# Performance work log

Hardware: AMD Instinct MI355X
Metric: run time of the kernel (lower is better)

The kernel has to match this reference:

```python
import jax, jax.numpy as jnp
import numpy as np
from jax.scipy.special import gammaln

# ---- constants matching init_kwargs ----
D = 64            # num_nodes
K = 64            # DiBS latent rank (k = d default)
P = 32            # n_particles
N_MC = 16         # MC graph samples for score-function grad estimator
PROJ = 128        # proj_dims
N = 2048          # observations
H = 5.0           # h_latent (Frobenius squared-exponential kernel bandwidth)
ALPHA = 0.2       # alpha_linear * t  (single SVGD step)
STEP = 0.005      # SVGD step size
ALPHA_MU = 1.0
ALPHA_LAMBD = float(D + 2)
THETA_MU = 0.0
P_EDGE = 4.0 / (D - 1)          # Erdos-Renyi edge prob (~2 expected edges/node)
LATENT_STD = 1.0 / np.sqrt(K)   # DiBS default latent prior std


def bge_log_marginal(g, data, mu0, alpha_mu, alpha_lambd):
    """BGe log marginal likelihood log p(data | G) for 0/1 adjacency g [d,d]."""
    n, d = data.shape
    small_t = alpha_mu * (alpha_lambd - d - 1.0) / (alpha_mu + 1.0)
    xbar = data.mean(0)
    xc = data - xbar
    R = small_t * jnp.eye(d) + xc.T @ xc \
        + (n * alpha_mu / (n + alpha_mu)) * jnp.outer(xbar - mu0, xbar - mu0)

    def masked_slogdet(mask):  # logdet of R restricted to mask-selected rows/cols
        m = jnp.outer(mask, mask)
        return jnp.linalg.slogdet(m * R + (1.0 - m) * jnp.eye(d))[1]

    def node_score(j):
        parents = g[:, j].astype(R.dtype)
        pj = jnp.maximum(parents, (jnp.arange(d) == j).astype(R.dtype))
        l = jnp.sum(parents)
        log_gamma = (0.5 * (jnp.log(alpha_mu) - jnp.log(n + alpha_mu))
                     + gammaln(0.5 * (n + alpha_lambd - d + l + 1.0))
                     - gammaln(0.5 * (alpha_lambd - d + l + 1.0))
                     - 0.5 * n * jnp.log(jnp.pi)
                     + 0.5 * (alpha_lambd - d + 2.0 * l + 1.0) * jnp.log(small_t))
        return (log_gamma
                + 0.5 * (n + alpha_lambd - d + l) * masked_slogdet(parents)
                - 0.5 * (n + alpha_lambd - d + l + 1.0) * masked_slogdet(pj))

    return jnp.sum(jax.vmap(node_score)(jnp.arange(d)))


def _dense(key, fan_in, fan_out):
    return jax.random.normal(key, (fan_in, fan_out), jnp.float32) * 0.05


def setup_inputs() -> dict:
    key = jax.random.key(0)
    ks = jax.random.split(key, 16)
    return {
        "z_gt": jax.random.normal(ks[0], (N, D), jnp.float32),
        "init_particles_z": jax.random.normal(ks[1], (P, D, K, 2), jnp.float32) * LATENT_STD,
        "enc_w0": _dense(ks[2], D * D, 20), "enc_b0": jnp.zeros(20, jnp.float32),
        "enc_w1": _dense(ks[3], 20, D),     "enc_b1": jnp.zeros(D, jnp.float32),
        "enc_w2": _dense(ks[4], D, D),      "enc_b2": jnp.zeros(D, jnp.float32),
        "mu_w0": _dense(ks[5], D, D), "mu_b0": jnp.zeros(D, jnp.float32),
        "mu_w1": _dense(ks[6], D, D), "mu_b1": jnp.zeros(D, jnp.float32),
        "lv_w0": _dense(ks[7], D, D), "lv_b0": jnp.zeros(D, jnp.float32),
        "lv_w1": _dense(ks[8], D, D), "lv_b1": jnp.zeros(D, jnp.float32),
        "dec_w0": _dense(ks[9], D, 10),       "dec_b0": jnp.zeros(10, jnp.float32),
        "dec_w1": _dense(ks[10], 10, PROJ),   "dec_b1": jnp.zeros(PROJ, jnp.float32),
        "dec_w2": _dense(ks[11], PROJ, PROJ), "dec_b2": jnp.zeros(PROJ, jnp.float32),
        "seed": 0,
    }


def reference(z_gt, init_particles_z, enc_w0, enc_b0, enc_w1, enc_b1, enc_w2, enc_b2,
              mu_w0, mu_b0, mu_w1, mu_b1, lv_w0, lv_b0, lv_w1, lv_b1,
              dec_w0, dec_b0, dec_w1, dec_b1, dec_w2, dec_b2, seed):
    key = jax.random.key(seed)
    d = z_gt.shape[1]
    od = 1.0 - jnp.eye(d)
    z = init_particles_z                                   # [P,d,k,2]
    u, v = z[..., 0], z[..., 1]
    scores = jnp.einsum('pik,pjk->pij', u, v)              # [P,d,d]
    probs = jax.nn.sigmoid(ALPHA * scores) * od            # soft graph, zero diag

    # --- score-function estimate of grad_z log E_G[p(data|G)] (DiBS marginal) ---
    key, sk = jax.random.split(key)
    gs = jax.random.bernoulli(sk, probs[:, None], (P, N_MC, d, d)).astype(z.dtype) * od
    mu0_inf = jnp.zeros(d, z.dtype)
    logp = jax.vmap(jax.vmap(
        lambda g: bge_log_marginal(g, z_gt, mu0_inf, 1.0, d + 2.0)))(gs)   # [P,S]
    w = jax.nn.softmax(logp, axis=1)                       # self-normalized weights
    M = ALPHA * (gs - probs[:, None]) * od                 # d log q(G|Z) / d scores
    grad_u = jnp.einsum('ps,psij,pjk->pik', w, M, v)
    grad_v = jnp.einsum('ps,psij,pik->pjk', w, M, u)

    # --- grad of soft-graph ER prior + Gaussian latent prior ---
    logit_pe = jnp.log(P_EDGE) - jnp.log1p(-P_EDGE)
    Mp = ALPHA * probs * (1.0 - probs) * logit_pe * od
    grad_u = grad_u + jnp.einsum('pij,pjk->pik', Mp, v) - u / (LATENT_STD ** 2)
    grad_v = grad_v + jnp.einsum('pij,pik->pjk', Mp, u) - v / (LATENT_STD ** 2)
    grads = jnp.stack([grad_u, grad_v], axis=-1)           # [P,d,k,2]

    # --- one SVGD step with Frobenius squared-exponential kernel ---
    zf = z.reshape(P, -1)
    gf = grads.reshape(P, -1)
    sq = jnp.sum((zf[:, None] - zf[None]) ** 2, -1)
    Kmat = jnp.exp(-sq / H)                                # symmetric [P,P]
    rep = (-2.0 / H) * (Kmat @ zf - zf * Kmat.sum(1, keepdims=True))
    z_new = z + STEP * ((Kmat @ gf + rep) / P).reshape(z.shape)

    # --- hard graphs: particle_to_g_lim (alpha -> inf) ---
    s2 = jnp.einsum('pik,pjk->pij', z_new[..., 0], z_new[..., 1])
    g_hard = (s2 > 0).astype(z.dtype) * od                 # [P,d,d]

    mu0_bge = jnp.full(d, THETA_MU, z.dtype)
    log_p_z_given_g = jax.vmap(
        lambda g: bge_log_marginal(g, z_gt, mu0_bge, ALPHA_MU, ALPHA_LAMBD))(g_hard)

    # --- q(z | G) encoder (batched over particles) ---
    gf2 = g_hard.reshape(g_hard.shape[0], d * d)
    h = jax.nn.relu(gf2 @ enc_w0 + enc_b0)
    h = jax.nn.relu(h @ enc_w1 + enc_b1)
    h = jax.nn.relu(h @ enc_w2 + enc_b2)
    q_mu = jax.nn.relu(h @ mu_w0 + mu_b0) @ mu_w1 + mu_b1
    q_lv = jax.nn.relu(h @ lv_w0 + lv_b0) @ lv_w1 + lv_b1

    key, rk = jax.random.split(key)
    eps = jax.random.normal(rk, q_lv.shape, q_lv.dtype)
    q_z = q_mu + eps * jnp.exp(0.5 * q_lv)                 # reparameterize

    # --- decoder ---
    hdec = jax.nn.relu(q_z @ dec_w0 + dec_b0)
    hdec = jax.nn.relu(hdec @ dec_w1 + dec_b1)
    recons = hdec @ dec_w2 + dec_b2                        # [P, PROJ]

    return recons, log_p_z_given_g, q_z, q_mu, q_lv, g_hard, z_new
```

## Files before the change

kernel.cpp:

```cpp
#include <hip/hip_runtime.h>
#include <stdint.h>
#include <math.h>

typedef unsigned long long u64;
typedef unsigned int u32;
typedef unsigned short u16;

#define C_P 32
#define C_S 16
#define C_D 64
#define C_N 2048

#define R_OFF      0
#define CTAB_OFF   4160
#define KEYS_OFF   4224
#define PROBS_OFF  4232
#define GROW_OFF   135304
#define GCOL_OFF   168072
#define NS_OFF     200840
#define W_OFF      233608
#define GF_OFF     234120
#define KM_OFF     365192
#define ZN_OFF     365704
#define NS2_OFF    496776

#define O_REC   0
#define O_LOGP  4096
#define O_QZ    4128
#define O_QMU   6176
#define O_QLV   8224
#define O_GH    10272
#define O_ZN    141344
#define O_TOTAL 403488

__device__ __forceinline__ void tf2x32(u32 k0, u32 k1, u32 x0, u32 x1,
                                       u32& o0, u32& o1) {
  u32 ks2 = k0 ^ k1 ^ 0x1BD11BDAu;
  x0 += k0; x1 += k1;
#define TFR(r) { x0 += x1; x1 = (x1 << r) | (x1 >> (32 - r)); x1 ^= x0; }
  TFR(13) TFR(15) TFR(26) TFR(6)   x0 += k1;  x1 += ks2 + 1u;
  TFR(17) TFR(29) TFR(16) TFR(24)  x0 += ks2; x1 += k0 + 2u;
  TFR(13) TFR(15) TFR(26) TFR(6)   x0 += k0;  x1 += k1 + 3u;
  TFR(17) TFR(29) TFR(16) TFR(24)  x0 += k1;  x1 += ks2 + 4u;
  TFR(13) TFR(15) TFR(26) TFR(6)   x0 += ks2; x1 += k0 + 5u;
#undef TFR
  o0 = x0; o1 = x1;
}

__device__ __forceinline__ double d_erfinv(double x) {
  double w = -log1p(-x * x);
  double p;
  if (w < 5.0) {
    w -= 2.5;
    p = 2.81022636e-08;
    p = 3.43273939e-07  + p * w;
    p = -3.5233877e-06  + p * w;
    p = -4.39150654e-06 + p * w;
    p = 0.00021858087   + p * w;
    p = -0.00125372503  + p * w;
    p = -0.00417768164  + p * w;
    p = 0.246640727     + p * w;
    p = 1.50140941      + p * w;
  } else {
    w = sqrt(w) - 3.0;
    p = -0.000200214257;
    p = 0.000100950558  + p * w;
    p = 0.00134934322   + p * w;
    p = -0.00367342844  + p * w;
    p = 0.00573950773   + p * w;
    p = -0.0076224613   + p * w;
    p = 0.00943887047   + p * w;
    p = 1.00167406      + p * w;
    p = 2.83297682      + p * w;
  }
  return p * x;
}

__global__ void k_R(const float* x, double* ws, const int* seedp) {
  __shared__ double pS[8][64], pX[8][64];
  __shared__ double xbar[64];
  int j = blockIdx.x, t = threadIdx.x;
  int i = t & 63, c = t >> 6;
  if (j == 0) {
    if (t < 64) {
      double l = (double)t;
      ws[CTAB_OFF + t] = -0.5 * log(2049.0)
                       + lgamma(0.5 * (2051.0 + l))
                       - lgamma(0.5 * (3.0 + l))
                       - 1024.0 * log(3.14159265358979323846)
                       + 0.5 * (2.0 * l + 3.0) * log(0.5);
    }
    if (t == 0) {
      u32 kk0 = 0u, kk1 = (u32)seedp[0];
      u32 a0, a1, s0, s1, r0, r1, d0, d1;
      tf2x32(kk0, kk1, 0u, 0u, a0, a1);
      tf2x32(kk0, kk1, 0u, 1u, s0, s1);
      tf2x32(a0, a1, 0u, 0u, d0, d1); (void)d0; (void)d1;
      tf2x32(a0, a1, 0u, 1u, r0, r1);
      u32* keys = (u32*)(ws + KEYS_OFF);
      keys[0] = s0; keys[1] = s1; keys[2] = r0; keys[3] = r1;
    }
  }
  double sx = 0.0, sxx = 0.0;
  for (int n = c * 256; n < (c + 1) * 256; n++) {
    double xi = (double)x[n * 64 + i];
    double xj = (double)x[n * 64 + j];
    sx += xi; sxx += xi * xj;
  }
  pS[c][i] = sx; pX[c][i] = sxx;
  __syncthreads();
  if (t < 64) {
    double S = 0.0, X = 0.0;
    for (int cc = 0; cc < 8; cc++) { S += pS[cc][i]; X += pX[cc][i]; }
    xbar[i] = S / 2048.0;
    pX[0][i] = X;
  }
  __syncthreads();
  if (t < 64) {
    double xbi = xbar[i], xbj = xbar[j];
    double s = pX[0][i] - 2048.0 * xbi * xbj + (2048.0 / 2049.0) * xbi * xbj;
    if (i == j) s += 0.5;
    ((float*)(ws + R_OFF))[i * 64 + j] = (float)s;
  }
}

__global__ __launch_bounds__(64) void k_probs(const float* z, double* ws) {
  float* probs = (float*)(ws + PROBS_OFF);
  int b = blockIdx.x; int p = b >> 6, i = b & 63;
  int j = threadIdx.x;
  __shared__ float V[64 * 65];
  __shared__ float us[64];
  int k = j;
  us[k] = z[((p * 64 + i) * 64 + k) * 2 + 0];
  for (int jj = 0; jj < 64; jj++)
    V[jj * 65 + k] = z[((p * 64 + jj) * 64 + k) * 2 + 1];
  __syncthreads();
  float s = 0.f;
  for (int kk = 0; kk < 64; kk++)
    s += us[kk] * V[j * 65 + kk];
  float pr = (i == j) ? 0.f : 1.f / (1.f + expf(-0.2f * s));
  probs[(p * 64 + i) * 64 + j] = pr;
}

__global__ void k_sample(double* ws) {
  const float* probs = (const float*)(ws + PROBS_OFF);
  const u32* keys = (const u32*)(ws + KEYS_OFF);
  u64* grow = (u64*)(ws + GROW_OFF);
  u64* gcol = (u64*)(ws + GCOL_OFF);
  int ps = blockIdx.x;
  int p = ps >> 4;
  int j = threadIdx.x;
  u32 k0 = keys[0], k1 = keys[1];
  u64 colmask = 0;
  for (int i = 0; i < 64; i++) {
    u32 lin = (u32)(ps * 4096 + i * 64 + j);
    u32 o0, o1; tf2x32(k0, k1, 0u, lin, o0, o1);
    u32 bits = o0 ^ o1;
    float f = __uint_as_float((bits >> 9) | 0x3f800000u) - 1.0f;
    bool bit = (f < probs[(p * 64 + i) * 64 + j]);
    u64 rm = __ballot(bit);
    if (j == 0) grow[ps * 64 + i] = rm;
    if (bit) colmask |= (1ull << i);
  }
  gcol[ps * 64 + j] = colmask;
}

__device__ __forceinline__ float rdlane(float x, int l) {
  return __uint_as_float(__builtin_amdgcn_readlane(__float_as_uint(x), (u32)l));
}

template<bool TRANSPOSE>
__global__ __launch_bounds__(64) void k_chol(const float* Rf, const double* ctab,
                                             const u64* masks, double* nodescore) {
  __shared__ float T[2080];
  __shared__ int idx[64];
  int task = blockIdx.x;
  int j = task & 63;
  int lane = threadIdx.x;
  u64 mask;
  if (TRANSPOSE) {
    int p = task >> 6;
    u64 rm = masks[p * 64 + lane];
    mask = __ballot((rm >> j) & 1ull);
  } else {
    mask = masks[task];
  }
  int P = (int)__popcll(mask);
  int m = P + 1;
  u64 below = mask & ((1ull << lane) - 1ull);
  if ((mask >> lane) & 1ull) idx[(int)__popcll(below)] = lane;
  if (lane == 0) idx[P] = j;
  __syncthreads();
  int trLane = (lane * (lane + 1)) >> 1;
  if (lane < m) {
    int cidx = idx[lane];
    int tr = 0;
    for (int r = 0; r < m; r++) {
      if (lane <= r) T[tr + lane] = Rf[idx[r] * 64 + cidx];
      tr += r + 1;
    }
  }
  __syncthreads();
  float mypiv = 1.0f, lastd = 1.0f;
  float v[40];
#pragma unroll
  for (int c = 0; c < 40; c++)
    v[c] = T[trLane + c];
#pragma unroll
  for (int k = 0; k < 40; k++) {
    if (k < m) {
      float dk = rdlane(v[k], k);
      if (lane == k) mypiv = dk;
      lastd = dk;
      float ns = -v[k] * __builtin_amdgcn_rcpf(dk);
#pragma unroll
      for (int b = k + 1; b < 40; b++)
        v[b] += ns * rdlane(v[k], b);
    }
  }
  if (m > 40) {
    for (int b = 40; b < m; b++) {
      float acc = 0.f;
#pragma unroll
      for (int k = 0; k < 40; k++) {
        float dk = rdlane(v[k], k);
        float abk = rdlane(v[k], b);
        acc += v[k] * abk * __builtin_amdgcn_rcpf(dk);
      }
      if (lane >= b) T[trLane + b] -= acc;
    }
    __syncthreads();
    for (int k = 40; k < m; k++) {
      float dk = T[((k * (k + 1)) >> 1) + k];
      if (lane == k) mypiv = dk;
      lastd = dk;
      float sk = T[trLane + k] * __builtin_amdgcn_rcpf(dk);
      for (int b = k + 1; b < m; b++) {
        float abk = T[((b * (b + 1)) >> 1) + k];
        if (lane >= b) T[trLane + b] -= sk * abk;
      }
      __syncthreads();
    }
  }
  double vv = (lane < m) ? log((double)mypiv) : 0.0;
  for (int off = 32; off > 0; off >>= 1) vv += __shfl_down(vv, off, 64);
  if (lane == 0) {
    double logB = vv;
    double logA = logB - log((double)lastd);
    double l = (double)P;
    nodescore[task] = ctab[P]
                    + 0.5 * (2050.0 + l) * logA
                    - 0.5 * (2051.0 + l) * logB;
  }
}

__global__ void k_logpw(const double* ns, double* w) {
  int p = blockIdx.x, t = threadIdx.x;
  __shared__ double part[64];
  int s = t & 15, c = t >> 4;
  double acc = 0.0;
  for (int j = c * 16; j < (c + 1) * 16; j++)
    acc += ns[(p * 16 + s) * 64 + j];
  part[t] = acc;
  __syncthreads();
  if (t < 16) part[t] = part[t] + part[t + 16] + part[t + 32] + part[t + 48];
  __syncthreads();
  if (t == 0) {
    double m = part[0];
    for (int s2 = 1; s2 < 16; s2++) m = fmax(m, part[s2]);
    double e[16], sum = 0.0;
    for (int s2 = 0; s2 < 16; s2++) { e[s2] = exp(part[s2] - m); sum += e[s2]; }
    for (int s2 = 0; s2 < 16; s2++) w[p * 16 + s2] = e[s2] / sum;
  }
}

__global__ void k_grad(double* ws, const float* z) {
  const float* probs = (const float*)(ws + PROBS_OFF);
  const double* w = ws + W_OFF;
  const u64* grow = (const u64*)(ws + GROW_OFF);
  const u64* gcol = (const u64*)(ws + GCOL_OFF);
  float* gf = (float*)(ws + GF_OFF);
  const float LOGIT = -2.6903717578966254f;
  int bb = blockIdx.x;
  int k = threadIdx.x;
  __shared__ float acc[64];
  if (bb < 2048) {
    int p = bb >> 6, i = bb & 63;
    float gb = 0.f, wsum = 0.f;
    for (int s = 0; s < 16; s++) {
      float wv = (float)w[p * 16 + s];
      wsum += wv;
      gb += wv * (float)((grow[(p * 16 + s) * 64 + i] >> k) & 1ull);
    }
    float pr = probs[(p * 64 + i) * 64 + k];
    float od = (i == k) ? 0.f : 1.f;
    acc[k] = (0.2f * (gb - pr * wsum) + 0.2f * pr * (1.f - pr) * LOGIT) * od;
    __syncthreads();
    float s = 0.f;
    for (int j = 0; j < 64; j++)
      s += acc[j] * z[((p * 64 + j) * 64 + k) * 2 + 1];
    s -= 64.f * z[((p * 64 + i) * 64 + k) * 2 + 0];
    gf[p * 8192 + (i * 64 + k) * 2 + 0] = s;
  } else if (bb < 4096) {
    int b = bb - 2048;
    int p = b >> 6, j = b & 63;
    float gb = 0.f, wsum = 0.f;
    for (int s = 0; s < 16; s++) {
      float wv = (float)w[p * 16 + s];
      wsum += wv;
      gb += wv * (float)((gcol[(p * 16 + s) * 64 + j] >> k) & 1ull);
    }
    float pr = probs[(p * 64 + k) * 64 + j];
    float od = (k == j) ? 0.f : 1.f;
    acc[k] = (0.2f * (gb - pr * wsum) + 0.2f * pr * (1.f - pr) * LOGIT) * od;
    __syncthreads();
    float s = 0.f;
    for (int i = 0; i < 64; i++)
      s += acc[i] * z[((p * 64 + i) * 64 + k) * 2 + 0];
    s -= 64.f * z[((p * 64 + j) * 64 + k) * 2 + 1];
    gf[p * 8192 + (j * 64 + k) * 2 + 1] = s;
  } else {
    float* Km = (float*)(ws + KM_OFF);
    int b = bb - 4096;
    int a = b >> 5, b2 = b & 31;
    float accf = 0.f;
    for (int d0 = k; d0 < 8192; d0 += 64) {
      float diff = z[a * 8192 + d0] - z[b2 * 8192 + d0];
      accf += diff * diff;
    }
    for (int off = 32; off > 0; off >>= 1) accf += __shfl_down(accf, off, 64);
    if (k == 0) Km[a * 32 + b2] = expf(-accf / 5.0f);
  }
}

__global__ void k_znew(const float* z, double* ws, float* out) {
  const float* Km = (const float*)(ws + KM_OFF);
  const float* gf = (const float*)(ws + GF_OFF);
  float* zn = (float*)(ws + ZN_OFF);
  int gid = blockIdx.x * 64 + threadIdx.x;
  int p = gid >> 13, t = gid & 8191;
  float zp = z[p * 8192 + t];
  float accg = 0.f, accz = 0.f, ks = 0.f;
  for (int b = 0; b < 32; b++) {
    float kv = Km[p * 32 + b];
    accg += kv * gf[b * 8192 + t];
    accz += kv * z[b * 8192 + t];
    ks += kv;
  }
  float rep = -0.4f * (accz - zp * ks);
  float v = zp + 0.005f * ((accg + rep) / 32.f);
  zn[p * 8192 + t] = v;
  out[O_ZN + p * 8192 + t] = v;
}

__global__ __launch_bounds__(64) void k_s2col(double* ws, float* out) {
  const float* zn = (const float*)(ws + ZN_OFF);
  u64* grow2 = (u64*)(ws + NS_OFF);
  int b = blockIdx.x; int p = b >> 6, i = b & 63;
  int j = threadIdx.x;
  __shared__ float V[64 * 65];
  __shared__ float us[64];
  int k = j;
  us[k] = zn[p * 8192 + (i * 64 + k) * 2 + 0];
  for (int jj = 0; jj < 64; jj++)
    V[jj * 65 + k] = zn[p * 8192 + (jj * 64 + k) * 2 + 1];
  __syncthreads();
  float s = 0.f;
  for (int kk = 0; kk < 64; kk++)
    s += us[kk] * V[j * 65 + kk];
  bool bit = (i != j) && (s > 0.0f);
  out[O_GH + (p * 64 + i) * 64 + j] = bit ? 1.0f : 0.0f;
  u64 m = __ballot(bit);
  if (j == 0) grow2[p * 64 + i] = m;
}

__global__ void k_mlp(double* ws, float* out, const double* ns2,
    const float* ew0, const float* eb0, const float* ew1, const float* eb1,
    const float* ew2, const float* eb2,
    const float* mw0, const float* mb0, const float* mw1, const float* mb1,
    const float* lw0, const float* lb0, const float* lw1, const float* lb1,
    const float* dw0, const float* db0, const float* dw1, const float* db1,
    const float* dw2, const float* db2) {
  int p = blockIdx.x, t = threadIdx.x;
  const u64* grow2 = (const u64*)(ws + NS_OFF);
  const u32* keys = (const u32*)(ws + KEYS_OFF);
  __shared__ float part[64][20];
  __shared__ float h0[20], h1[64], h2[64], hm[64], hl[64];
  __shared__ float qmu[64], qlv[64], qz[64], h3[10], h4[128];
  __shared__ u64 gc[64];
  {
    double vv = ns2[p * 64 + t];
    for (int off = 32; off > 0; off >>= 1) vv += __shfl_down(vv, off, 64);
    if (t == 0) out[O_LOGP + p] = (float)vv;
  }
  {
    u64 cmask = 0;
    for (int i = 0; i < 64; i++)
      cmask |= ((grow2[p * 64 + i] >> t) & 1ull) << i;
    gc[t] = cmask;
  }
  __syncthreads();
  {
    float acc[20];
#pragma unroll
    for (int o = 0; o < 20; o++) acc[o] = 0.f;
    u64 m = gc[t];
    for (int i = 0; i < 64; i++) {
      float msk = (float)((m >> i) & 1ull);
      const float* wr = ew0 + (i * 64 + t) * 20;
#pragma unroll
      for (int o = 0; o < 20; o++) acc[o] += msk * wr[o];
    }
    for (int o = 0; o < 20; o++) part[t][o] = acc[o];
  }
  __syncthreads();
  if (t < 20) {
    float s = eb0[t];
    for (int q = 0; q < 64; q++) s += part[q][t];
    h0[t] = fmaxf(s, 0.f);
  }
  __syncthreads();
  {
    float s = eb1[t];
    for (int q = 0; q < 20; q++) s += h0[q] * ew1[q * 64 + t];
    h1[t] = fmaxf(s, 0.f);
  }
  __syncthreads();
  {
    float s = eb2[t];
    for (int q = 0; q < 64; q++) s += h1[q] * ew2[q * 64 + t];
    h2[t] = fmaxf(s, 0.f);
  }
  __syncthreads();
  {
    float s = mb0[t];
    for (int q = 0; q < 64; q++) s += h2[q] * mw0[q * 64 + t];
    hm[t] = fmaxf(s, 0.f);
    float s2 = lb0[t];
    for (int q = 0; q < 64; q++) s2 += h2[q] * lw0[q * 64 + t];
    hl[t] = fmaxf(s2, 0.f);
  }
  __syncthreads();
  {
    float s = mb1[t];
    for (int q = 0; q < 64; q++) s += hm[q] * mw1[q * 64 + t];
    qmu[t] = s;
    float s2 = lb1[t];
    for (int q = 0; q < 64; q++) s2 += hl[q] * lw1[q * 64 + t];
    qlv[t] = s2;
  }
  {
    u32 o0, o1;
    tf2x32(keys[2], keys[3], 0u, (u32)(p * 64 + t), o0, o1);
    u32 bits = o0 ^ o1;
    float f = __uint_as_float((bits >> 9) | 0x3f800000u) - 1.0f;
    float LOF = __uint_as_float(0xBF7FFFFFu);
    float uu = fmaxf(LOF, f * 2.0f + LOF);
    float eps = (float)(1.4142135623730951 * d_erfinv((double)uu));
    float qzv = qmu[t] + eps * expf(0.5f * qlv[t]);
    qz[t] = qzv;
    out[O_QZ  + p * 64 + t] = qzv;
    out[O_QMU + p * 64 + t] = qmu[t];
    out[O_QLV + p * 64 + t] = qlv[t];
  }
  __syncthreads();
  if (t < 10) {
    float s = db0[t];
    for (int q = 0; q < 64; q++) s += qz[q] * dw0[q * 10 + t];
    h3[t] = fmaxf(s, 0.f);
  }
  __syncthreads();
  for (int o = t; o < 128; o += 64) {
    float s = db1[o];
    for (int q = 0; q < 10; q++) s += h3[q] * dw1[q * 128 + o];
    h4[o] = fmaxf(s, 0.f);
  }
  __syncthreads();
  for (int o = t; o < 128; o += 64) {
    float s = db2[o];
    for (int q = 0; q < 128; q++) s += h4[q] * dw2[q * 128 + o];
    out[O_REC + p * 128 + o] = s;
  }
}

extern "C" void kernel_launch(void* const* d_in, const int* in_sizes, int n_in,
                              void* d_out, int out_size, void* d_ws, size_t ws_size,
                              hipStream_t stream) {
  (void)in_sizes; (void)n_in; (void)out_size; (void)ws_size;
  const float* z_gt = (const float*)d_in[0];
  const float* z0   = (const float*)d_in[1];
  const float* ew0 = (const float*)d_in[2];  const float* eb0 = (const float*)d_in[3];
  const float* ew1 = (const float*)d_in[4];  const float* eb1 = (const float*)d_in[5];
  const float* ew2 = (const float*)d_in[6];  const float* eb2 = (const float*)d_in[7];
  const float* mw0 = (const float*)d_in[8];  const float* mb0 = (const float*)d_in[9];
  const float* mw1 = (const float*)d_in[10]; const float* mb1 = (const float*)d_in[11];
  const float* lw0 = (const float*)d_in[12]; const float* lb0 = (const float*)d_in[13];
  const float* lw1 = (const float*)d_in[14]; const float* lb1 = (const float*)d_in[15];
  const float* dw0 = (const float*)d_in[16]; const float* db0 = (const float*)d_in[17];
  const float* dw1 = (const float*)d_in[18]; const float* db1 = (const float*)d_in[19];
  const float* dw2 = (const float*)d_in[20]; const float* db2 = (const float*)d_in[21];
  const int* seed = (const int*)d_in[22];
  double* ws = (double*)d_ws;
  float* out = (float*)d_out;
  const float* Rf = (const float*)(ws + R_OFF);

  k_R<<<64, 512, 0, stream>>>(z_gt, ws, seed);
  k_probs<<<C_P * C_D, 64, 0, stream>>>(z0, ws);
  k_sample<<<C_P * C_S, 64, 0, stream>>>(ws);
  k_chol<false><<<C_P * C_S * C_D, 64, 0, stream>>>(Rf, ws + CTAB_OFF,
      (const u64*)(ws + GCOL_OFF), ws + NS_OFF);
  k_logpw<<<C_P, 64, 0, stream>>>(ws + NS_OFF, ws + W_OFF);
  k_grad<<<2 * C_P * C_D + C_P * C_P, 64, 0, stream>>>(ws, z0);
  k_znew<<<(C_P * 8192) / 64, 64, 0, stream>>>(z0, ws, out);
  k_s2col<<<C_P * C_D, 64, 0, stream>>>(ws, out);
  k_chol<true><<<C_P * C_D, 64, 0, stream>>>(Rf, ws + CTAB_OFF,
      (const u64*)(ws + NS_OFF), ws + NS2_OFF);
  k_mlp<<<C_P, 64, 0, stream>>>(ws, out, ws + NS2_OFF,
      ew0, eb0, ew1, eb1, ew2, eb2,
      mw0, mb0, mw1, mb1, lw0, lb0, lw1, lb1,
      dw0, db0, dw1, db1, dw2, db2);
}
```

Before: 378.9 us.

## Split MC-sample Cholesky into light register-LDL kernel and heavy overflow kernel

```diff
diff --git a/kernel.cpp b/kernel.cpp
--- a/kernel.cpp
+++ b/kernel.cpp
@@ -150,6 +150,7 @@
   int ps = blockIdx.x;
   int p = ps >> 4;
   int j = threadIdx.x;
+  if (ps == 0 && j == 0) ((u32*)(ws + GF_OFF))[0] = 0;
   u32 k0 = keys[0], k1 = keys[1];
   u64 colmask = 0;
   for (int i = 0; i < 64; i++) {
@@ -167,6 +168,159 @@
 
 __device__ __forceinline__ float rdlane(float x, int l) {
   return __uint_as_float(__builtin_amdgcn_readlane(__float_as_uint(x), (u32)l));
+}
+
+template<int MMAX>
+__device__ __forceinline__ void ldl_core(const float* T, int tb, int lane, int m,
+                                         float& mypiv, float& lastd) {
+  float v[MMAX];
+#pragma unroll
+  for (int c = 0; c < MMAX; c++)
+    v[c] = T[tb + c];
+#pragma unroll
+  for (int k = 0; k < MMAX; k++) {
+    if (k < m) {
+      float dk = rdlane(v[k], k);
+      if (lane == k) mypiv = dk;
+      lastd = dk;
+      float ns = -v[k] * __builtin_amdgcn_rcpf(dk);
+#pragma unroll
+      for (int b = k + 1; b < MMAX; b++)
+        v[b] += ns * rdlane(v[k], b);
+    }
+  }
+}
+
+__global__ __launch_bounds__(128, 8) void k_chol_light(const float* Rf, const double* ctab,
+                                                       const u64* masks, double* nodescore,
+                                                       u32* heavy) {
+  __shared__ float T[2][820];
+  __shared__ int idx[2][64];
+  int w = threadIdx.x >> 6;
+  int lane = threadIdx.x & 63;
+  int task = blockIdx.x * 2 + w;
+  int j = task & 63;
+  u64 mask = masks[task];
+  int P = (int)__popcll(mask);
+  int m = P + 1;
+  bool heavyTask = (m > 40);
+  if (heavyTask) {
+    if (lane == 0) {
+      u32 slot = atomicAdd(heavy, 1u);
+      heavy[1 + slot] = (u32)task;
+    }
+    m = 1; P = 0;
+  }
+  u64 below = mask & ((1ull << lane) - 1ull);
+  if (!heavyTask && ((mask >> lane) & 1ull)) idx[w][(int)__popcll(below)] = lane;
+  if (lane == 0) idx[w][P] = j;
+  __syncthreads();
+  int trLane = (lane * (lane + 1)) >> 1;
+  if (lane < m) {
+    int cidx = idx[w][lane];
+    int tr = 0;
+    for (int r = 0; r < m; r++) {
+      if (lane <= r) T[w][tr + lane] = Rf[idx[w][r] * 64 + cidx];
+      tr += r + 1;
+    }
+  }
+  __syncthreads();
+  float mypiv = 1.0f, lastd = 1.0f;
+  int tb = (lane < 40) ? trLane : 0;
+  if (m <= 34) ldl_core<34>(T[w], tb, lane, m, mypiv, lastd);
+  else         ldl_core<40>(T[w], tb, lane, m, mypiv, lastd);
+  double vv = (lane < m) ? log((double)mypiv) : 0.0;
+  for (int off = 32; off > 0; off >>= 1) vv += __shfl_down(vv, off, 64);
+  if (lane == 0 && !heavyTask) {
+    double logB = vv;
+    double logA = logB - log((double)lastd);
+    double l = (double)P;
+    nodescore[task] = ctab[P]
+                    + 0.5 * (2050.0 + l) * logA
+                    - 0.5 * (2051.0 + l) * logB;
+  }
+}
+
+__global__ __launch_bounds__(64) void k_chol_heavy(const float* Rf, const double* ctab,
+                                                   const u64* masks, double* nodescore,
+                                                   const u32* heavy) {
+  __shared__ float T[2080];
+  __shared__ int idx[64];
+  int lane = threadIdx.x;
+  u32 cnt = heavy[0];
+  for (u32 ii = blockIdx.x; ii < cnt; ii += gridDim.x) {
+    __syncthreads();
+    int task = (int)heavy[1 + ii];
+    int j = task & 63;
+    u64 mask = masks[task];
+    int P = (int)__popcll(mask);
+    int m = P + 1;
+    u64 below = mask & ((1ull << lane) - 1ull);
+    if ((mask >> lane) & 1ull) idx[(int)__popcll(below)] = lane;
+    if (lane == 0) idx[P] = j;
+    __syncthreads();
+    int trLane = (lane * (lane + 1)) >> 1;
+    if (lane < m) {
+      int cidx = idx[lane];
+      int tr = 0;
+      for (int r = 0; r < m; r++) {
+        if (lane <= r) T[tr + lane] = Rf[idx[r] * 64 + cidx];
+        tr += r + 1;
+      }
+    }
+    __syncthreads();
+    float mypiv = 1.0f, lastd = 1.0f;
+    float v[40];
+#pragma unroll
+    for (int c = 0; c < 40; c++)
+      v[c] = T[trLane + c];
+#pragma unroll
+    for (int k = 0; k < 40; k++) {
+      if (k < m) {
+        float dk = rdlane(v[k], k);
+        if (lane == k) mypiv = dk;
+        lastd = dk;
+        float ns = -v[k] * __builtin_amdgcn_rcpf(dk);
+#pragma unroll
+        for (int b = k + 1; b < 40; b++)
+          v[b] += ns * rdlane(v[k], b);
+      }
+    }
+    if (m > 40) {
+      for (int b = 40; b < m; b++) {
+        float acc = 0.f;
+#pragma unroll
+        for (int k = 0; k < 40; k++) {
+          float dk = rdlane(v[k], k);
+          float abk = rdlane(v[k], b);
+          acc += v[k] * abk * __builtin_amdgcn_rcpf(dk);
+        }
+        if (lane >= b) T[trLane + b] -= acc;
+      }
+      __syncthreads();
+      for (int k = 40; k < m; k++) {
+        float dk = T[((k * (k + 1)) >> 1) + k];
+        if (lane == k) mypiv = dk;
+        lastd = dk;
+        float sk = T[trLane + k] * __builtin_amdgcn_rcpf(dk);
+        for (int b = k + 1; b < m; b++) {
+          float abk = T[((b * (b + 1)) >> 1) + k];
+          if (lane >= b) T[trLane + b] -= sk * abk;
+        }
+        __syncthreads();
+      }
+    }
+    double vv = (lane < m) ? log((double)mypiv) : 0.0;
+    for (int off = 32; off > 0; off >>= 1) vv += __shfl_down(vv, off, 64);
+    if (lane == 0) {
+      double logB = vv;
+      double logA = logB - log((double)lastd);
+      double l = (double)P;
+      nodescore[task] = ctab[P]
+                      + 0.5 * (2050.0 + l) * logA
+                      - 0.5 * (2051.0 + l) * logB;
+    }
+  }
 }
 
 template<bool TRANSPOSE>
@@ -503,12 +657,15 @@
   double* ws = (double*)d_ws;
   float* out = (float*)d_out;
   const float* Rf = (const float*)(ws + R_OFF);
+  u32* heavy = (u32*)(ws + GF_OFF);
 
   k_R<<<64, 512, 0, stream>>>(z_gt, ws, seed);
   k_probs<<<C_P * C_D, 64, 0, stream>>>(z0, ws);
   k_sample<<<C_P * C_S, 64, 0, stream>>>(ws);
-  k_chol<false><<<C_P * C_S * C_D, 64, 0, stream>>>(Rf, ws + CTAB_OFF,
-      (const u64*)(ws + GCOL_OFF), ws + NS_OFF);
+  k_chol_light<<<(C_P * C_S * C_D) / 2, 128, 0, stream>>>(Rf, ws + CTAB_OFF,
+      (const u64*)(ws + GCOL_OFF), ws + NS_OFF, heavy);
+  k_chol_heavy<<<1024, 64, 0, stream>>>(Rf, ws + CTAB_OFF,
+      (const u64*)(ws + GCOL_OFF), ws + NS_OFF, heavy);
   k_logpw<<<C_P, 64, 0, stream>>>(ws + NS_OFF, ws + W_OFF);
   k_grad<<<2 * C_P * C_D + C_P * C_P, 64, 0, stream>>>(ws, z0);
   k_znew<<<(C_P * 8192) / 64, 64, 0, stream>>>(z0, ws, out);
```

Measured after the change: 439.5 us. 16.0% more time.
